# Performance work log

Measured on AMD Instinct MI355X. Metric: run time of the kernel, lower is better.

Reference implementation:

```python
import jax, jax.numpy as jnp
import numpy as np

EPS = 1e-8


def _vq(feats, E):
    # feats: (B, L, 3), E: (V, 3)
    B, L, D = feats.shape
    flat = feats.reshape(-1, D)
    dist = (flat ** 2).sum(1, keepdims=True) - 2.0 * flat @ E.T + (E ** 2).sum(1)
    idx = jnp.argmin(dist, axis=1)
    quant = E[idx].reshape(B, L, D)
    sg = jax.lax.stop_gradient
    loss = jnp.mean((quant - sg(feats)) ** 2) + 0.25 * jnp.mean((feats - sg(quant)) ** 2)
    quant_st = feats + sg(quant - feats)  # straight-through
    return quant_st, idx.reshape(B, L), loss


def _high_tokens(h, scale):
    # h: (B, C, O, H, W, 2) -> tokens (B, H*W*O*C, 3)
    real, imag = h[..., 0], h[..., 1]
    amp = jnp.sqrt(real ** 2 + imag ** 2)
    mean = amp.mean(axis=(1, 2, 3, 4))
    std = amp.std(axis=(1, 2, 3, 4), ddof=1) + EPS  # torch std is unbiased
    amp_n = (amp - mean[:, None, None, None, None]) / std[:, None, None, None, None] * scale
    cos = real / (amp + EPS)
    sin = imag / (amp + EPS)
    q = jnp.stack((amp_n, cos, sin), axis=-1)            # (B,C,O,H,W,3)
    q = q.transpose(0, 3, 4, 2, 1, 5)                    # (B,H,W,O,C,3)
    return q.reshape(q.shape[0], -1, 3)


def _low_tokens(yl, scale):
    # yl: (B, C, H, W) -> tokens (B, H*W*1*C, 3)
    amp = jnp.abs(yl)
    mean = amp.mean(axis=(1, 2, 3))
    std = amp.std(axis=(1, 2, 3), ddof=1) + EPS
    amp_n = (amp - mean[:, None, None, None]) / std[:, None, None, None] * scale
    cos = yl / (amp + EPS)
    sin = jnp.zeros_like(yl)
    q = jnp.stack((amp_n, cos, sin), axis=-1)[:, :, None]  # (B,C,1,H,W,3)
    q = q.transpose(0, 3, 4, 2, 1, 5)                      # (B,H,W,1,C,3)
    return q.reshape(q.shape[0], -1, 3)


def setup_inputs() -> dict:
    key = jax.random.key(0)
    ks = jax.random.split(key, 6)
    B, C, O = 2, 3, 6
    V, D = 4096, 3
    yh0 = jax.random.normal(ks[0], (B, C, O, 64, 64, 2), dtype=jnp.float32)
    yh1 = jax.random.normal(ks[1], (B, C, O, 32, 32, 2), dtype=jnp.float32)
    yh2 = jax.random.normal(ks[2], (B, C, O, 16, 16, 2), dtype=jnp.float32)
    yl = jax.random.normal(ks[3], (B, C, 16, 16), dtype=jnp.float32)
    bound = float(np.sqrt(6.0 / (V + D)))  # xavier_uniform
    emb_weight = jax.random.uniform(ks[4], (V, D), minval=-bound, maxval=bound, dtype=jnp.float32)
    level_scale = jnp.ones((4,), dtype=jnp.float32)
    return {"yh0": yh0, "yh1": yh1, "yh2": yh2, "yl": yl,
            "emb_weight": emb_weight, "level_scale": level_scale}


def reference(yh0, yh1, yh2, yl, emb_weight, level_scale):
    quants, idxs = [], []
    loss = jnp.float32(0.0)
    for li, h in enumerate((yh0, yh1, yh2)):
        tok = _high_tokens(h, level_scale[li])
        q, idx, l = _vq(tok, emb_weight)
        quants.append(q)
        idxs.append(idx)
        loss = loss + l
    tok = _low_tokens(yl, level_scale[-1])
    q, idx, l = _vq(tok, emb_weight)
    quants.append(q)
    idxs.append(idx)
    loss = loss + l
    quant_all = jnp.concatenate(quants, axis=1)  # (B, L_total, 3)
    idx_all = jnp.concatenate(idxs, axis=1)      # (B, L_total)
    return quant_all, idx_all, loss
```

## Files before the change

kernel.cpp:

```cpp
#include <hip/hip_runtime.h>
#include <math.h>

namespace {
constexpr int CC = 3, OO = 6, VV = 4096;
constexpr int W0 = 64, W1 = 32, W2 = 16, WL = 16;
constexpr int L0 = W0 * W0 * OO * CC;
constexpr int L1 = W1 * W1 * OO * CC;
constexpr int L2 = W2 * W2 * OO * CC;
constexpr int LLOW = WL * WL * CC;
constexpr int LT = L0 + L1 + L2 + LLOW;
constexpr int NTOK = 2 * LT;
constexpr int BS = 256;
constexpr int NBLK = NTOK / BS;
constexpr int CH = 8192;
static_assert(NTOK % BS == 0, "grid must tile exactly");
}

__global__ __launch_bounds__(256) void stats_kernel(const float* __restrict__ yh0,
                                                    const float* __restrict__ yh1,
                                                    const float* __restrict__ yh2,
                                                    const float* __restrict__ yl,
                                                    float* __restrict__ statsf) {
#pragma clang fp contract(off)
  __shared__ alignas(16) float lds[2 * CH];
  __shared__ float sh_mean;
  int grp = blockIdx.x, level = grp >> 1, b = grp & 1;
  const float* src;
  int N;
  bool cplx = (level < 3);
  if (level == 0)      { src = yh0 + (size_t)b * L0 * 2; N = L0; }
  else if (level == 1) { src = yh1 + (size_t)b * L1 * 2; N = L1; }
  else if (level == 2) { src = yh2 + (size_t)b * L2 * 2; N = L2; }
  else                 { src = yl + (size_t)b * LLOW;    N = LLOW; }
  int tid = threadIdx.x;
  int nchunks = (N + CH - 1) / CH;

  auto amp_at = [&](int e) -> float {
#pragma clang fp contract(off)
    if (cplx) {
      float re = src[2 * e], im = src[2 * e + 1];
      return __fsqrt_rn(fmaf(re, re, __fmul_rn(im, im)));
    }
    return fabsf(src[e]);
  };

  auto stage = [&](int c, int pass, float mean, int first, int step) {
#pragma clang fp contract(off)
    if (tid < first) return;
    int off = c * CH;
    int cnt = min(CH, N - off);
    float* dst = &lds[(c & 1) * CH];
    for (int j = tid - first; j < cnt; j += step) {
      float a = amp_at(off + j);
      if (pass) a = __fsub_rn(a, mean);
      dst[j] = a;
    }
  };

  auto fold_sum = [&](int c, float& s) {
#pragma clang fp contract(off)
    const float4* lb = (const float4*)&lds[(c & 1) * CH];
    int nv = min(CH, N - c * CH) >> 2;
    float4 A[8], B[8];
#pragma unroll
    for (int p = 0; p < 8; ++p) A[p] = lb[p];
    int iters = nv >> 4;
    for (int it = 0; it < iters; ++it) {
      const int i = it << 4;
#pragma unroll
      for (int p = 0; p < 8; ++p) B[p] = lb[i + 8 + p];
#pragma unroll
      for (int p = 0; p < 8; ++p) {
        s = __fadd_rn(s, A[p].x);
        s = __fadd_rn(s, A[p].y);
        s = __fadd_rn(s, A[p].z);
        s = __fadd_rn(s, A[p].w);
      }
      if (it + 1 < iters) {
#pragma unroll
        for (int p = 0; p < 8; ++p) A[p] = lb[i + 16 + p];
      }
#pragma unroll
      for (int p = 0; p < 8; ++p) {
        s = __fadd_rn(s, B[p].x);
        s = __fadd_rn(s, B[p].y);
        s = __fadd_rn(s, B[p].z);
        s = __fadd_rn(s, B[p].w);
      }
    }
  };

  auto fold_sq = [&](int c, float& s) {
#pragma clang fp contract(off)
    const float4* lb = (const float4*)&lds[(c & 1) * CH];
    int nv = min(CH, N - c * CH) >> 2;
    float4 A[8], B[8];
#pragma unroll
    for (int p = 0; p < 8; ++p) A[p] = lb[p];
    int iters = nv >> 4;
    for (int it = 0; it < iters; ++it) {
      const int i = it << 4;
#pragma unroll
      for (int p = 0; p < 8; ++p) B[p] = lb[i + 8 + p];
#pragma unroll
      for (int p = 0; p < 8; ++p) {
        s = fmaf(A[p].x, A[p].x, s);
        s = fmaf(A[p].y, A[p].y, s);
        s = fmaf(A[p].z, A[p].z, s);
        s = fmaf(A[p].w, A[p].w, s);
      }
      if (it + 1 < iters) {
#pragma unroll
        for (int p = 0; p < 8; ++p) A[p] = lb[i + 16 + p];
      }
#pragma unroll
      for (int p = 0; p < 8; ++p) {
        s = fmaf(B[p].x, B[p].x, s);
        s = fmaf(B[p].y, B[p].y, s);
        s = fmaf(B[p].z, B[p].z, s);
        s = fmaf(B[p].w, B[p].w, s);
      }
    }
  };

  float s = 0.0f;
  stage(0, 0, 0.0f, 0, BS);
  __syncthreads();
  for (int c = 0; c < nchunks; ++c) {
    if (c + 1 < nchunks) stage(c + 1, 0, 0.0f, 64, BS - 64);
    if (tid == 0) fold_sum(c, s);
    __syncthreads();
  }
  if (tid == 0) sh_mean = __fdiv_rn(s, (float)N);
  __syncthreads();
  float mean = sh_mean;

  float ss = 0.0f;
  stage(0, 1, mean, 0, BS);
  __syncthreads();
  for (int c = 0; c < nchunks; ++c) {
    if (c + 1 < nchunks) stage(c + 1, 1, mean, 64, BS - 64);
    if (tid == 0) fold_sq(c, ss);
    __syncthreads();
  }
  if (tid == 0) {
    float var = __fdiv_rn(ss, (float)(N - 1));
    statsf[grp] = mean;
    statsf[8 + grp] = __fadd_rn(__fsqrt_rn(var), 1e-8f);
  }
}


__global__ void cb_kernel(const float* __restrict__ emb, float4* __restrict__ cbf) {
  int v = blockIdx.x * BS + threadIdx.x;
  if (v < VV) {
    float e0 = emb[3 * v], e1 = emb[3 * v + 1], e2 = emb[3 * v + 2];
    float es = __fadd_rn(__fadd_rn(__fmul_rn(e0, e0), __fmul_rn(e1, e1)),
                         __fmul_rn(e2, e2));
    cbf[v] = make_float4(e0, e1, e2, es);
  }
}

__global__ __launch_bounds__(256) void vq_kernel(
    const float* __restrict__ yh0, const float* __restrict__ yh1,
    const float* __restrict__ yh2, const float* __restrict__ yl,
    const float* __restrict__ emb, const float* __restrict__ scl,
    const float4* __restrict__ cbf, const float* __restrict__ statsf,
    float* __restrict__ out_quant, float* __restrict__ out_idx,
    double* __restrict__ part) {
  __shared__ float4 cb[VV];
  for (int v = threadIdx.x; v < VV; v += BS) cb[v] = cbf[v];

  int g = blockIdx.x * BS + threadIdx.x;
  int b = g / LT;
  int t = g - b * LT;
  int level;
  float f0, f1, f2;
  if (t < L0 + L1 + L2) {
    const float* src;
    int Wd, r;
    if (t < L0)           { level = 0; r = t;           Wd = W0; src = yh0; }
    else if (t < L0 + L1) { level = 1; r = t - L0;      Wd = W1; src = yh1; }
    else                  { level = 2; r = t - L0 - L1; Wd = W2; src = yh2; }
    int c = r % CC;
    int r2 = r / CC;
    int o = r2 % OO;
    int r3 = r2 / OO;
    int x = r3 % Wd;
    int y = r3 / Wd;
    size_t base = ((((size_t)b * CC + c) * OO + o) * Wd + y) * Wd + x;
    float re = src[2 * base], im = src[2 * base + 1];
    float amp = __fsqrt_rn(__fadd_rn(__fmul_rn(re, re), __fmul_rn(im, im)));
    float mean = statsf[2 * level + b];
    float sdep = statsf[8 + 2 * level + b];
    f0 = __fmul_rn(__fdiv_rn(__fsub_rn(amp, mean), sdep), scl[level]);
    float den = __fadd_rn(amp, 1e-8f);
    f1 = __fdiv_rn(re, den);
    f2 = __fdiv_rn(im, den);
  } else {
    level = 3;
    int r = t - (L0 + L1 + L2);
    int c = r % CC;
    int xy = r / CC;
    int x = xy % WL;
    int y = xy / WL;
    size_t base = (((size_t)b * CC + c) * WL + y) * WL + x;
    float v = yl[base];
    float amp = fabsf(v);
    f0 = __fmul_rn(__fdiv_rn(__fsub_rn(amp, statsf[6 + b]), statsf[14 + b]), scl[3]);
    f1 = __fdiv_rn(v, __fadd_rn(amp, 1e-8f));
    f2 = 0.0f;
  }

  float fsum = __fadd_rn(__fadd_rn(__fmul_rn(f0, f0), __fmul_rn(f1, f1)),
                         __fmul_rn(f2, f2));
  __syncthreads();
  float best = INFINITY;
  int bi = 0;
#pragma unroll 4
  for (int v = 0; v < VV; ++v) {
    float4 e = cb[v];
    float fe = fmaf(f2, e.z, fmaf(f1, e.y, __fmul_rn(f0, e.x)));
    float dist = __fadd_rn(__fsub_rn(fsum, __fadd_rn(fe, fe)), e.w);
    if (dist < best) { best = dist; bi = v; }
  }

  float q0 = emb[3 * bi], q1 = emb[3 * bi + 1], q2 = emb[3 * bi + 2];
  float d0 = __fsub_rn(q0, f0), d1 = __fsub_rn(q1, f1), d2 = __fsub_rn(q2, f2);
  out_quant[3 * g + 0] = __fadd_rn(f0, d0);
  out_quant[3 * g + 1] = __fadd_rn(f1, d1);
  out_quant[3 * g + 2] = __fadd_rn(f2, d2);
  out_idx[g] = (float)bi;

  double sse = (double)d0 * d0 + (double)d1 * d1 + (double)d2 * d2;
  __shared__ double sh[BS];
  for (int l = 0; l < 4; ++l) {
    sh[threadIdx.x] = (level == l) ? sse : 0.0;
    __syncthreads();
    for (int off = BS / 2; off > 0; off >>= 1) {
      if ((int)threadIdx.x < off) sh[threadIdx.x] += sh[threadIdx.x + off];
      __syncthreads();
    }
    if (threadIdx.x == 0) part[4 * blockIdx.x + l] = sh[0];
    __syncthreads();
  }
}

__global__ void finalize_kernel(const double* __restrict__ part, float* __restrict__ out_loss) {
  double s[4] = {0.0, 0.0, 0.0, 0.0};
  for (int i = threadIdx.x; i < NBLK; i += BS)
    for (int l = 0; l < 4; ++l) s[l] += part[4 * i + l];
  __shared__ double sh[BS];
  __shared__ double tot;
  if (threadIdx.x == 0) tot = 0.0;
  const double cnt[4] = {2.0 * L0 * 3, 2.0 * L1 * 3, 2.0 * L2 * 3, 2.0 * LLOW * 3};
  for (int l = 0; l < 4; ++l) {
    sh[threadIdx.x] = s[l];
    __syncthreads();
    for (int off = BS / 2; off > 0; off >>= 1) {
      if ((int)threadIdx.x < off) sh[threadIdx.x] += sh[threadIdx.x + off];
      __syncthreads();
    }
    if (threadIdx.x == 0) tot += 1.25 * sh[0] / cnt[l];
    __syncthreads();
  }
  if (threadIdx.x == 0) out_loss[0] = (float)tot;
}

extern "C" void kernel_launch(void* const* d_in, const int* in_sizes, int n_in,
                              void* d_out, int out_size, void* d_ws, size_t ws_size,
                              hipStream_t stream) {
  const float* yh0 = (const float*)d_in[0];
  const float* yh1 = (const float*)d_in[1];
  const float* yh2 = (const float*)d_in[2];
  const float* yl = (const float*)d_in[3];
  const float* emb = (const float*)d_in[4];
  const float* scl = (const float*)d_in[5];

  float* out = (float*)d_out;
  float* out_quant = out;
  float* out_idx = out + 3 * NTOK;
  float* out_loss = out + 4 * NTOK;

  float4* cbf = (float4*)d_ws;
  float* statsf = (float*)((char*)d_ws + 65536);
  double* part = (double*)((char*)d_ws + 65600);

  hipLaunchKernelGGL(cb_kernel, dim3(VV / BS), dim3(BS), 0, stream, emb, cbf);
  hipLaunchKernelGGL(stats_kernel, dim3(8), dim3(BS), 0, stream, yh0, yh1, yh2, yl, statsf);
  hipLaunchKernelGGL(vq_kernel, dim3(NBLK), dim3(BS), 0, stream,
                     yh0, yh1, yh2, yl, emb, scl, cbf, statsf, out_quant, out_idx, part);
  hipLaunchKernelGGL(finalize_kernel, dim3(1), dim3(BS), 0, stream, part, out_loss);
}
```

Measured before the change: 833.7 us.

## Fuse codebook prep into VQ kernel, prescale features, restructure stats folds

Removes the separate codebook kernel and builds the float4 codebook (with squared norm) directly in shared memory in each VQ block. The features are premultiplied by two so the inner distance loop drops one add, and that loop is unrolled by 8 instead of 4. The quantized vector is read from shared memory rather than global, and the stats fold loops are restructured to interleave loads with the adds and peel the last iteration. Each block now recomputes the codebook norms from strided global loads, adding work per block in exchange for one fewer launch.

```diff
diff --git a/kernel.cpp b/kernel.cpp
--- a/kernel.cpp
+++ b/kernel.cpp
@@ -61,65 +61,91 @@
 #pragma clang fp contract(off)
     const float4* lb = (const float4*)&lds[(c & 1) * CH];
     int nv = min(CH, N - c * CH) >> 2;
+    int nw = nv >> 4;
     float4 A[8], B[8];
 #pragma unroll
     for (int p = 0; p < 8; ++p) A[p] = lb[p];
-    int iters = nv >> 4;
-    for (int it = 0; it < iters; ++it) {
-      const int i = it << 4;
-#pragma unroll
-      for (int p = 0; p < 8; ++p) B[p] = lb[i + 8 + p];
+    int w = 0;
+    for (; w + 1 < nw; ++w) {
+      const int i = w << 4;
 #pragma unroll
       for (int p = 0; p < 8; ++p) {
+        B[p] = lb[i + 8 + p];
         s = __fadd_rn(s, A[p].x);
         s = __fadd_rn(s, A[p].y);
         s = __fadd_rn(s, A[p].z);
         s = __fadd_rn(s, A[p].w);
       }
-      if (it + 1 < iters) {
-#pragma unroll
-        for (int p = 0; p < 8; ++p) A[p] = lb[i + 16 + p];
-      }
 #pragma unroll
       for (int p = 0; p < 8; ++p) {
+        A[p] = lb[i + 16 + p];
         s = __fadd_rn(s, B[p].x);
         s = __fadd_rn(s, B[p].y);
         s = __fadd_rn(s, B[p].z);
         s = __fadd_rn(s, B[p].w);
       }
     }
+    const int i = w << 4;
+#pragma unroll
+    for (int p = 0; p < 8; ++p) {
+      B[p] = lb[i + 8 + p];
+      s = __fadd_rn(s, A[p].x);
+      s = __fadd_rn(s, A[p].y);
+      s = __fadd_rn(s, A[p].z);
+      s = __fadd_rn(s, A[p].w);
+    }
+#pragma unroll
+    for (int p = 0; p < 8; ++p) {
+      s = __fadd_rn(s, B[p].x);
+      s = __fadd_rn(s, B[p].y);
+      s = __fadd_rn(s, B[p].z);
+      s = __fadd_rn(s, B[p].w);
+    }
   };
 
   auto fold_sq = [&](int c, float& s) {
 #pragma clang fp contract(off)
     const float4* lb = (const float4*)&lds[(c & 1) * CH];
     int nv = min(CH, N - c * CH) >> 2;
+    int nw = nv >> 4;
     float4 A[8], B[8];
 #pragma unroll
     for (int p = 0; p < 8; ++p) A[p] = lb[p];
-    int iters = nv >> 4;
-    for (int it = 0; it < iters; ++it) {
-      const int i = it << 4;
-#pragma unroll
-      for (int p = 0; p < 8; ++p) B[p] = lb[i + 8 + p];
+    int w = 0;
+    for (; w + 1 < nw; ++w) {
+      const int i = w << 4;
 #pragma unroll
       for (int p = 0; p < 8; ++p) {
+        B[p] = lb[i + 8 + p];
         s = fmaf(A[p].x, A[p].x, s);
         s = fmaf(A[p].y, A[p].y, s);
         s = fmaf(A[p].z, A[p].z, s);
         s = fmaf(A[p].w, A[p].w, s);
       }
-      if (it + 1 < iters) {
-#pragma unroll
-        for (int p = 0; p < 8; ++p) A[p] = lb[i + 16 + p];
-      }
 #pragma unroll
       for (int p = 0; p < 8; ++p) {
+        A[p] = lb[i + 16 + p];
         s = fmaf(B[p].x, B[p].x, s);
         s = fmaf(B[p].y, B[p].y, s);
         s = fmaf(B[p].z, B[p].z, s);
         s = fmaf(B[p].w, B[p].w, s);
       }
+    }
+    const int i = w << 4;
+#pragma unroll
+    for (int p = 0; p < 8; ++p) {
+      B[p] = lb[i + 8 + p];
+      s = fmaf(A[p].x, A[p].x, s);
+      s = fmaf(A[p].y, A[p].y, s);
+      s = fmaf(A[p].z, A[p].z, s);
+      s = fmaf(A[p].w, A[p].w, s);
+    }
+#pragma unroll
+    for (int p = 0; p < 8; ++p) {
+      s = fmaf(B[p].x, B[p].x, s);
+      s = fmaf(B[p].y, B[p].y, s);
+      s = fmaf(B[p].z, B[p].z, s);
+      s = fmaf(B[p].w, B[p].w, s);
     }
   };
 
@@ -150,26 +176,23 @@
   }
 }
 
-
-__global__ void cb_kernel(const float* __restrict__ emb, float4* __restrict__ cbf) {
-  int v = blockIdx.x * BS + threadIdx.x;
-  if (v < VV) {
-    float e0 = emb[3 * v], e1 = emb[3 * v + 1], e2 = emb[3 * v + 2];
-    float es = __fadd_rn(__fadd_rn(__fmul_rn(e0, e0), __fmul_rn(e1, e1)),
-                         __fmul_rn(e2, e2));
-    cbf[v] = make_float4(e0, e1, e2, es);
-  }
-}
-
 __global__ __launch_bounds__(256) void vq_kernel(
     const float* __restrict__ yh0, const float* __restrict__ yh1,
     const float* __restrict__ yh2, const float* __restrict__ yl,
     const float* __restrict__ emb, const float* __restrict__ scl,
-    const float4* __restrict__ cbf, const float* __restrict__ statsf,
+    const float* __restrict__ statsf,
     float* __restrict__ out_quant, float* __restrict__ out_idx,
     double* __restrict__ part) {
   __shared__ float4 cb[VV];
-  for (int v = threadIdx.x; v < VV; v += BS) cb[v] = cbf[v];
+  {
+#pragma clang fp contract(off)
+    for (int v = threadIdx.x; v < VV; v += BS) {
+      float e0 = emb[3 * v], e1 = emb[3 * v + 1], e2 = emb[3 * v + 2];
+      float es = __fadd_rn(__fadd_rn(__fmul_rn(e0, e0), __fmul_rn(e1, e1)),
+                           __fmul_rn(e2, e2));
+      cb[v] = make_float4(e0, e1, e2, es);
+    }
+  }
 
   int g = blockIdx.x * BS + threadIdx.x;
   int b = g / LT;
@@ -214,19 +237,20 @@
 
   float fsum = __fadd_rn(__fadd_rn(__fmul_rn(f0, f0), __fmul_rn(f1, f1)),
                          __fmul_rn(f2, f2));
+  float m0 = __fmul_rn(f0, 2.0f), m1 = __fmul_rn(f1, 2.0f), m2 = __fmul_rn(f2, 2.0f);
   __syncthreads();
   float best = INFINITY;
   int bi = 0;
-#pragma unroll 4
+#pragma unroll 8
   for (int v = 0; v < VV; ++v) {
     float4 e = cb[v];
-    float fe = fmaf(f2, e.z, fmaf(f1, e.y, __fmul_rn(f0, e.x)));
-    float dist = __fadd_rn(__fsub_rn(fsum, __fadd_rn(fe, fe)), e.w);
+    float fe2 = fmaf(m2, e.z, fmaf(m1, e.y, __fmul_rn(m0, e.x)));
+    float dist = __fadd_rn(__fsub_rn(fsum, fe2), e.w);
     if (dist < best) { best = dist; bi = v; }
   }
 
-  float q0 = emb[3 * bi], q1 = emb[3 * bi + 1], q2 = emb[3 * bi + 2];
-  float d0 = __fsub_rn(q0, f0), d1 = __fsub_rn(q1, f1), d2 = __fsub_rn(q2, f2);
+  float4 q = cb[bi];
+  float d0 = __fsub_rn(q.x, f0), d1 = __fsub_rn(q.y, f1), d2 = __fsub_rn(q.z, f2);
   out_quant[3 * g + 0] = __fadd_rn(f0, d0);
   out_quant[3 * g + 1] = __fadd_rn(f1, d1);
   out_quant[3 * g + 2] = __fadd_rn(f2, d2);
@@ -282,13 +306,11 @@
   float* out_idx = out + 3 * NTOK;
   float* out_loss = out + 4 * NTOK;
 
-  float4* cbf = (float4*)d_ws;
-  float* statsf = (float*)((char*)d_ws + 65536);
-  double* part = (double*)((char*)d_ws + 65600);
-
-  hipLaunchKernelGGL(cb_kernel, dim3(VV / BS), dim3(BS), 0, stream, emb, cbf);
+  float* statsf = (float*)d_ws;
+  double* part = (double*)((char*)d_ws + 128);
+
   hipLaunchKernelGGL(stats_kernel, dim3(8), dim3(BS), 0, stream, yh0, yh1, yh2, yl, statsf);
   hipLaunchKernelGGL(vq_kernel, dim3(NBLK), dim3(BS), 0, stream,
-                     yh0, yh1, yh2, yl, emb, scl, cbf, statsf, out_quant, out_idx, part);
+                     yh0, yh1, yh2, yl, emb, scl, statsf, out_quant, out_idx, part);
   hipLaunchKernelGGL(finalize_kernel, dim3(1), dim3(BS), 0, stream, part, out_loss);
 }
```

Result: faster. 802.6 us (-3.7%).
